# Optimization experiments

Hardware: AMD Instinct MI355X
Metric: run time of the kernel (lower is better)

The kernel has to match this reference:

```python
import jax, jax.numpy as jnp
import numpy as np

# Model dims (match init_kwargs)
NUM_EXPERTS = 8
TOP_K = 2
D_MODEL = 1024
D_FF = 4096
BATCH = 4
SEQ = 2048


def setup_inputs() -> dict:
    key = jax.random.key(0)
    ks = jax.random.split(key, 6)
    x = jax.random.normal(ks[0], (BATCH, SEQ, D_MODEL), dtype=jnp.float32)
    # Linear gating network: logits = x @ Wg + bg
    Wg = jax.random.normal(ks[1], (D_MODEL, NUM_EXPERTS), dtype=jnp.float32) * (D_MODEL ** -0.5)
    bg = jnp.zeros((NUM_EXPERTS,), dtype=jnp.float32)
    # Per-expert 2-layer FFN params, stacked over expert axis E
    W1 = jax.random.normal(ks[2], (NUM_EXPERTS, D_MODEL, D_FF), dtype=jnp.float32) * (D_MODEL ** -0.5)
    b1 = jnp.zeros((NUM_EXPERTS, D_FF), dtype=jnp.float32)
    W2 = jax.random.normal(ks[3], (NUM_EXPERTS, D_FF, D_MODEL), dtype=jnp.float32) * (D_FF ** -0.5)
    b2 = jnp.zeros((NUM_EXPERTS, D_MODEL), dtype=jnp.float32)
    return {"x": x, "Wg": Wg, "bg": bg, "W1": W1, "b1": b1, "W2": W2, "b2": b2}


def reference(x, Wg, bg, W1, b1, W2, b2):
    B, S, D = x.shape
    E = Wg.shape[1]
    xf = x.reshape(-1, D)  # [T, D], T = B*S tokens

    # --- Linear gating: softmax probs, top-k hard assignment mask ---
    gate_logits = xf @ Wg + bg                      # [T, E]
    gate_probs = jax.nn.softmax(gate_logits, -1)    # [T, E]
    _, top_idx = jax.lax.top_k(gate_probs, TOP_K)   # [T, K]
    # expert_assignment = sum over k of one_hot(indices) -> {0,1} mask [T, E]
    assign = jnp.sum(jax.nn.one_hot(top_idx, E, dtype=gate_probs.dtype), axis=-2)

    # --- All experts process all tokens (faithful to _process_hard_routing) ---
    # h: [E, T, F]; out_e: [E, T, D]
    h = jax.nn.gelu(jnp.einsum('td,edf->etf', xf, W1) + b1[:, None, :])
    out_e = jnp.einsum('etf,efd->etd', h, W2) + b2[:, None, :]

    # --- Weighted combine: expert_output * gate_prob * top-k mask, sum over E ---
    w = (gate_probs * assign).T[:, :, None]         # [E, T, 1]
    out = jnp.sum(out_e * w, axis=0)                # [T, D]
    return out.reshape(B, S, D)
```

## Files before the change

kernel.cpp:

```cpp
#include <hip/hip_runtime.h>
#include <hip/hip_bf16.h>
#include <stdint.h>

#define T_TOK 8192
#define DM 1024
#define DF 4096
#define NE 8
#define NSLOT 136

typedef __attribute__((ext_vector_type(8))) short short8;
typedef __attribute__((ext_vector_type(8))) unsigned short ushort8;
typedef __attribute__((ext_vector_type(4))) float f32x4;

#define AS1 __attribute__((address_space(1)))
#define AS3 __attribute__((address_space(3)))

#define NB_GATE (T_TOK / 4)
#define NB_T1 ((DF / 64) * (DM / 64) * NE)
#define NB_T2 ((DM / 64) * (DF / 64) * NE)

static __device__ __forceinline__ unsigned short f2bf(float f) {
  union { float f; unsigned int u; } c; c.f = f;
  unsigned int u = c.u;
  unsigned int r = (u + 0x7FFFu + ((u >> 16) & 1u)) >> 16;
  return (unsigned short)r;
}

static __device__ __forceinline__ float gelu_tanh(float v) {
  float y = 0.7978845608028654f * (v + 0.044715f * v * v * v);
  float ay = fabsf(y);
  float e = __expf(-2.0f * ay);
  float th = (1.0f - e) / (1.0f + e);
  th = copysignf(th, y);
  return 0.5f * v * (1.0f + th);
}

__global__ void k_probe(float* out, float v, int n) {
  int i = blockIdx.x * blockDim.x + threadIdx.x;
  for (; i < n; i += gridDim.x * blockDim.x) out[i] = v;
}

__global__ void k_prep(const float* __restrict__ x, unsigned short* __restrict__ xb,
                       const float* __restrict__ Wg, const float* __restrict__ bg,
                       const float* __restrict__ W1, unsigned short* __restrict__ w1t,
                       const float* __restrict__ W2, unsigned short* __restrict__ w2t,
                       const float* __restrict__ b2, float* __restrict__ out,
                       int* __restrict__ choice2, float* __restrict__ wts) {
  __shared__ float tile[64][65];
  int bid = blockIdx.x;

  if (bid < NB_GATE) {
    int wave = threadIdx.x >> 6, lane = threadIdx.x & 63;
    int t = bid * 4 + wave;
    const float* xr = x + (size_t)t * DM;
    unsigned short* xo = xb + (size_t)t * DM;
    double acc[NE];
#pragma unroll
    for (int e = 0; e < NE; ++e) acc[e] = 0.0;
#pragma unroll
    for (int i = 0; i < 4; ++i) {
      int d = lane * 4 + i * 256;
      float4 v = *(const float4*)(xr + d);
      ushort4 o;
      o.x = f2bf(v.x); o.y = f2bf(v.y); o.z = f2bf(v.z); o.w = f2bf(v.w);
      *(ushort4*)(xo + d) = o;
      float xv[4] = {v.x, v.y, v.z, v.w};
#pragma unroll
      for (int q = 0; q < 4; ++q) {
        const float4* wg = (const float4*)(Wg + (size_t)(d + q) * NE);
        float4 w0 = wg[0], w1 = wg[1];
        acc[0] += (double)xv[q] * w0.x; acc[1] += (double)xv[q] * w0.y;
        acc[2] += (double)xv[q] * w0.z; acc[3] += (double)xv[q] * w0.w;
        acc[4] += (double)xv[q] * w1.x; acc[5] += (double)xv[q] * w1.y;
        acc[6] += (double)xv[q] * w1.z; acc[7] += (double)xv[q] * w1.w;
      }
    }
#pragma unroll
    for (int off = 32; off; off >>= 1)
#pragma unroll
      for (int e = 0; e < NE; ++e) acc[e] += __shfl_xor(acc[e], off);
    int e1i = 0, e2i = 0;
    float w1v = 0.f, w2v = 0.f;
    if (lane == 0) {
      float lg[NE];
#pragma unroll
      for (int e = 0; e < NE; ++e) lg[e] = (float)acc[e] + bg[e];
      float m = lg[0];
#pragma unroll
      for (int e = 1; e < NE; ++e) m = fmaxf(m, lg[e]);
      float s = 0.f, p[NE];
#pragma unroll
      for (int e = 0; e < NE; ++e) { p[e] = expf(lg[e] - m); s += p[e]; }
      float inv = 1.f / s;
      int i1 = 0;
#pragma unroll
      for (int e = 1; e < NE; ++e) if (lg[e] > lg[i1]) i1 = e;
      int i2 = (i1 == 0) ? 1 : 0;
#pragma unroll
      for (int e = 0; e < NE; ++e) if (e != i1 && lg[e] > lg[i2]) i2 = e;
      e1i = i1; e2i = i2;
      w1v = p[i1] * inv; w2v = p[i2] * inv;
      choice2[2 * t] = i1;     wts[2 * t] = w1v;
      choice2[2 * t + 1] = i2; wts[2 * t + 1] = w2v;
    }
    e1i = __shfl(e1i, 0); e2i = __shfl(e2i, 0);
    w1v = __shfl(w1v, 0); w2v = __shfl(w2v, 0);
#pragma unroll
    for (int i = 0; i < 4; ++i) {
      int d = lane * 4 + i * 256;
      float4 a = *(const float4*)(b2 + (size_t)e1i * DM + d);
      float4 b = *(const float4*)(b2 + (size_t)e2i * DM + d);
      float4 o;
      o.x = w1v * a.x + w2v * b.x; o.y = w1v * a.y + w2v * b.y;
      o.z = w1v * a.z + w2v * b.z; o.w = w1v * a.w + w2v * b.w;
      *(float4*)(out + (size_t)t * DM + d) = o;
    }
    return;
  }

  const float* src;
  unsigned short* dst;
  int R, C, r0, c0;
  if (bid < NB_GATE + NB_T1) {
    int b2i = bid - NB_GATE;
    int e = b2i >> 10, rem = b2i & 1023;
    int byy = rem >> 6, bxx = rem & 63;
    R = DM; C = DF; r0 = byy * 64; c0 = bxx * 64;
    src = W1 + (size_t)e * DM * DF;
    dst = w1t + (size_t)e * DM * DF;
  } else {
    int b2i = bid - NB_GATE - NB_T1;
    int e = b2i >> 10, rem = b2i & 1023;
    int byy = rem >> 4, bxx = rem & 15;
    R = DF; C = DM; r0 = byy * 64; c0 = bxx * 64;
    src = W2 + (size_t)e * DF * DM;
    dst = w2t + (size_t)e * DF * DM;
  }
  int tx = threadIdx.x & 15, ty = threadIdx.x >> 4;
#pragma unroll
  for (int i = 0; i < 4; ++i) {
    int r = ty + i * 16;
    float4 v = *(const float4*)(src + (size_t)(r0 + r) * C + c0 + tx * 4);
    tile[r][tx * 4 + 0] = v.x; tile[r][tx * 4 + 1] = v.y;
    tile[r][tx * 4 + 2] = v.z; tile[r][tx * 4 + 3] = v.w;
  }
  __syncthreads();
  int tx2 = threadIdx.x & 7, ty2 = threadIdx.x >> 3;
#pragma unroll
  for (int i = 0; i < 2; ++i) {
    int c = ty2 + i * 32;
    ushort8 o;
#pragma unroll
    for (int j = 0; j < 8; ++j) o[j] = f2bf(tile[tx2 * 8 + j][c]);
    *(ushort8*)(dst + (size_t)(c0 + c) * R + r0 + tx2 * 8) = o;
  }
}

__global__ void k_bucket(const int* __restrict__ choice2, const float* __restrict__ wts,
                         int* __restrict__ counts, int* __restrict__ offsets,
                         int* __restrict__ btok, float* __restrict__ bw,
                         int* __restrict__ work) {
  __shared__ int qc[4][NE];
  int e = blockIdx.x;
  int tid = threadIdx.x;
  int w = tid >> 6, lane = tid & 63;
  const int QUARTER = 2 * T_TOK / 4;
  int base = w * QUARTER;
  unsigned long long below = (lane == 0) ? 0ull : ((1ull << lane) - 1ull);

  int cq[NE];
#pragma unroll
  for (int q = 0; q < NE; ++q) cq[q] = 0;
  for (int i0 = 0; i0 < QUARTER; i0 += 64) {
    int ce = choice2[base + i0 + lane];
#pragma unroll
    for (int q = 0; q < NE; ++q)
      cq[q] += (int)__popcll(__ballot(ce == q));
  }
  if (lane == 0) {
#pragma unroll
    for (int q = 0; q < NE; ++q) qc[w][q] = cq[q];
  }
  __syncthreads();

  int total[NE];
#pragma unroll
  for (int q = 0; q < NE; ++q) total[q] = qc[0][q] + qc[1][q] + qc[2][q] + qc[3][q];
  int off_e = 0;
#pragma unroll
  for (int q = 0; q < NE; ++q) if (q < e) off_e += total[q];
  int pos = 0;
#pragma unroll
  for (int ww = 0; ww < 4; ++ww) if (ww < w) pos += qc[ww][e];

  if (e == 0 && tid == 0) {
    int s = 0;
    for (int q = 0; q < NE; ++q) { counts[q] = total[q]; offsets[q] = s; s += total[q]; }
    int idx = 0;
    for (int q = 0; q < NE; ++q) {
      int nby = (total[q] + 127) >> 7;
      for (int j = 0; j < nby; ++j) work[idx++] = (q << 20) | (j << 7);
    }
    while (idx < NSLOT) work[idx++] = -1;
  }

  for (int i0 = 0; i0 < QUARTER; i0 += 64) {
    int idx = base + i0 + lane;
    int ce = choice2[idx];
    float wt = wts[idx];
    unsigned long long m = __ballot(ce == e);
    if (ce == e) {
      int r = (int)__popcll(m & below);
      btok[e * T_TOK + pos + r] = idx >> 1;
      bw[e * T_TOK + pos + r] = wt;
    }
    pos += (int)__popcll(m);
  }
}


__global__ __launch_bounds__(256, 4) void k_gemm1(
    const unsigned short* __restrict__ xb,
    const unsigned short* __restrict__ w1t,
    const float* __restrict__ b1,
    const int* __restrict__ counts, const int* __restrict__ offsets,
    const int* __restrict__ btok, const int* __restrict__ work,
    unsigned short* __restrict__ H,
    int gx) {
  __shared__ __align__(16) unsigned short ldsA[128 * 64];
  __shared__ __align__(16) unsigned short ldsB[128 * 64];
  __shared__ int toksh[128];

  int nwg = gx * NSLOT;
  int bid = blockIdx.x;
  int wg = (bid & 7) * (nwg >> 3) + (bid >> 3);
  int slot = wg / gx;
  int bx = wg - slot * gx;
  int pk = work[slot];
  if (pk < 0) return;
  int e = pk >> 20;
  int m0 = pk & 0xFFFFF;
  int cnt = counts[e];
  int eoff = offsets[e];
  int f0 = bx * 128;
  int tid = threadIdx.x;
  int wave = tid >> 6, lane = tid & 63;

  for (int i = tid; i < 128; i += 256) {
    int p = m0 + i; if (p >= cnt) p = cnt - 1;
    toksh[i] = btok[e * T_TOK + p];
  }
  __syncthreads();

  int slin = lane & 7, rsub = lane >> 3;
  int ksl8 = (slin ^ rsub) * 8;

  const unsigned short* srcA[4];
  const unsigned short* srcB[4];
  int ldsg[4];
#pragma unroll
  for (int j = 0; j < 4; ++j) {
    int g = j * 4 + wave;
    int m = g * 8 + rsub;
    srcA[j] = xb + (size_t)toksh[m] * DM + ksl8;
    srcB[j] = w1t + ((size_t)e * DF + f0 + m) * DM + ksl8;
    ldsg[j] = g * 512;
  }

  auto stage = [&](int ks) {
#pragma unroll
    for (int j = 0; j < 4; ++j) {
      __builtin_amdgcn_global_load_lds((const AS1 void*)(srcA[j] + (size_t)ks * 64),
                                       (AS3 void*)(&ldsA[ldsg[j]]), 16, 0, 0);
      __builtin_amdgcn_global_load_lds((const AS1 void*)(srcB[j] + (size_t)ks * 64),
                                       (AS3 void*)(&ldsB[ldsg[j]]), 16, 0, 0);
    }
  };

  int wm = wave >> 1, wn = wave & 1;
  int lrow = lane & 15, khi = lane >> 4;
  f32x4 acc[4][4];
#pragma unroll
  for (int m = 0; m < 4; ++m)
#pragma unroll
    for (int n = 0; n < 4; ++n) acc[m][n] = (f32x4){0.f, 0.f, 0.f, 0.f};

  auto compute = [&]() {
#pragma unroll
    for (int kk = 0; kk < 2; ++kk) {
      int kslot = kk * 4 + khi;
      short8 af[4], bfv[4];
#pragma unroll
      for (int m = 0; m < 4; ++m) {
        int row = wm * 64 + m * 16 + lrow;
        int slotx = kslot ^ (row & 7);
        af[m] = *(const short8*)(&ldsA[row * 64 + slotx * 8]);
      }
#pragma unroll
      for (int n = 0; n < 4; ++n) {
        int row = wn * 64 + n * 16 + lrow;
        int slotx = kslot ^ (row & 7);
        bfv[n] = *(const short8*)(&ldsB[row * 64 + slotx * 8]);
      }
#pragma unroll
      for (int m = 0; m < 4; ++m)
#pragma unroll
        for (int n = 0; n < 4; ++n)
          acc[m][n] = __builtin_amdgcn_mfma_f32_16x16x32_bf16(af[m], bfv[n], acc[m][n], 0, 0, 0);
    }
  };

  const int nk = DM / 64;
  for (int ks = 0; ks < nk; ++ks) {
    stage(ks);
    __syncthreads();
    compute();
    __syncthreads();
  }

#pragma unroll
  for (int m = 0; m < 4; ++m) {
    int rbase = wm * 64 + m * 16 + khi * 4;
#pragma unroll
    for (int j = 0; j < 4; ++j) {
      int pos = m0 + rbase + j;
      if (pos < cnt) {
        size_t hrow = (size_t)(eoff + pos) * DF;
#pragma unroll
        for (int n = 0; n < 4; ++n) {
          int fl = f0 + wn * 64 + n * 16 + lrow;
          float v = acc[m][n][j] + b1[e * DF + fl];
          H[hrow + fl] = f2bf(gelu_tanh(v));
        }
      }
    }
  }
}

__global__ __launch_bounds__(256, 4) void k_gemm2(
    const unsigned short* __restrict__ H,
    const unsigned short* __restrict__ w2t,
    const int* __restrict__ counts, const int* __restrict__ offsets,
    const int* __restrict__ btok, const float* __restrict__ bw,
    const int* __restrict__ work,
    float* __restrict__ out, int gx) {
  __shared__ __align__(16) unsigned short ldsA[128 * 64];
  __shared__ __align__(16) unsigned short ldsB[128 * 64];
  __shared__ int toksh[128];
  __shared__ float wsh[128];

  int nwg = gx * NSLOT;
  int bid = blockIdx.x;
  int wg = (bid & 7) * (nwg >> 3) + (bid >> 3);
  int slot = wg / gx;
  int bx = wg - slot * gx;
  int pk = work[slot];
  if (pk < 0) return;
  int e = pk >> 20;
  int m0 = pk & 0xFFFFF;
  int cnt = counts[e];
  int eoff = offsets[e];
  int d0 = bx * 128;
  int tid = threadIdx.x;
  int wave = tid >> 6, lane = tid & 63;

  for (int i = tid; i < 128; i += 256) {
    int p = m0 + i; if (p >= cnt) p = cnt - 1;
    toksh[i] = btok[e * T_TOK + p];
    wsh[i] = bw[e * T_TOK + p];
  }
  __syncthreads();

  int slin = lane & 7, rsub = lane >> 3;
  int ksl8 = (slin ^ rsub) * 8;

  const unsigned short* srcA[4];
  const unsigned short* srcB[4];
  int ldsg[4];
#pragma unroll
  for (int j = 0; j < 4; ++j) {
    int g = j * 4 + wave;
    int m = g * 8 + rsub;
    int p = m0 + m; if (p >= cnt) p = cnt - 1;
    srcA[j] = H + (size_t)(eoff + p) * DF + ksl8;
    srcB[j] = w2t + ((size_t)e * DM + d0 + m) * DF + ksl8;
    ldsg[j] = g * 512;
  }

  auto stage = [&](int ks) {
#pragma unroll
    for (int j = 0; j < 4; ++j) {
      __builtin_amdgcn_global_load_lds((const AS1 void*)(srcA[j] + (size_t)ks * 64),
                                       (AS3 void*)(&ldsA[ldsg[j]]), 16, 0, 0);
      __builtin_amdgcn_global_load_lds((const AS1 void*)(srcB[j] + (size_t)ks * 64),
                                       (AS3 void*)(&ldsB[ldsg[j]]), 16, 0, 0);
    }
  };

  int wm = wave >> 1, wn = wave & 1;
  int lrow = lane & 15, khi = lane >> 4;
  f32x4 acc[4][4];
#pragma unroll
  for (int m = 0; m < 4; ++m)
#pragma unroll
    for (int n = 0; n < 4; ++n) acc[m][n] = (f32x4){0.f, 0.f, 0.f, 0.f};

  auto compute = [&]() {
#pragma unroll
    for (int kk = 0; kk < 2; ++kk) {
      int kslot = kk * 4 + khi;
      short8 af[4], bfv[4];
#pragma unroll
      for (int m = 0; m < 4; ++m) {
        int row = wm * 64 + m * 16 + lrow;
        int slotx = kslot ^ (row & 7);
        af[m] = *(const short8*)(&ldsA[row * 64 + slotx * 8]);
      }
#pragma unroll
      for (int n = 0; n < 4; ++n) {
        int row = wn * 64 + n * 16 + lrow;
        int slotx = kslot ^ (row & 7);
        bfv[n] = *(const short8*)(&ldsB[row * 64 + slotx * 8]);
      }
#pragma unroll
      for (int m = 0; m < 4; ++m)
#pragma unroll
        for (int n = 0; n < 4; ++n)
          acc[m][n] = __builtin_amdgcn_mfma_f32_16x16x32_bf16(af[m], bfv[n], acc[m][n], 0, 0, 0);
    }
  };

  const int nk = DF / 64;
  for (int ks = 0; ks < nk; ++ks) {
    stage(ks);
    __syncthreads();
    compute();
    __syncthreads();
  }

#pragma unroll
  for (int m = 0; m < 4; ++m) {
    int rbase = wm * 64 + m * 16 + khi * 4;
#pragma unroll
    for (int j = 0; j < 4; ++j) {
      int lr = rbase + j;
      int pos = m0 + lr;
      if (pos < cnt) {
        int tok = toksh[lr];
        float wgt = wsh[lr];
#pragma unroll
        for (int n = 0; n < 4; ++n) {
          int dc = d0 + wn * 64 + n * 16 + lrow;
          atomicAdd(&out[(size_t)tok * DM + dc], wgt * acc[m][n][j]);
        }
      }
    }
  }
}

extern "C" void kernel_launch(void* const* d_in, const int* in_sizes, int n_in,
                              void* d_out, int out_size, void* d_ws, size_t ws_size,
                              hipStream_t stream) {
  const float* x  = (const float*)d_in[0];
  const float* Wg = (const float*)d_in[1];
  const float* bg = (const float*)d_in[2];
  const float* W1 = (const float*)d_in[3];
  const float* b1 = (const float*)d_in[4];
  const float* W2 = (const float*)d_in[5];
  const float* b2 = (const float*)d_in[6];
  float* out = (float*)d_out;

  uint8_t* ws = (uint8_t*)d_ws;
  size_t off = 0;
  auto alloc = [&](size_t bytes) {
    size_t o = off;
    off = (off + bytes + 255) & ~(size_t)255;
    return o;
  };
  size_t o_counts = alloc(NE * 4);
  size_t o_offsets = alloc(NE * 4);
  size_t o_work = alloc(NSLOT * 4);
  size_t o_choice = alloc((size_t)2 * T_TOK * 4);
  size_t o_wts = alloc((size_t)2 * T_TOK * 4);
  size_t o_btok = alloc((size_t)NE * T_TOK * 4);
  size_t o_bw = alloc((size_t)NE * T_TOK * 4);
  size_t o_xb = alloc((size_t)T_TOK * DM * 2);
  size_t o_w1t = alloc((size_t)NE * DF * DM * 2);
  size_t o_w2t = alloc((size_t)NE * DM * DF * 2);
  size_t o_h = alloc((size_t)2 * T_TOK * DF * 2);

  if (off > ws_size) {
    k_probe<<<dim3(1024), dim3(256), 0, stream>>>(out, (float)(double)ws_size, out_size);
    return;
  }

  int* counts = (int*)(ws + o_counts);
  int* offsets = (int*)(ws + o_offsets);
  int* work = (int*)(ws + o_work);
  int* choice2 = (int*)(ws + o_choice);
  float* wtsp = (float*)(ws + o_wts);
  int* btok = (int*)(ws + o_btok);
  float* bwp = (float*)(ws + o_bw);
  unsigned short* xb = (unsigned short*)(ws + o_xb);
  unsigned short* w1t = (unsigned short*)(ws + o_w1t);
  unsigned short* w2t = (unsigned short*)(ws + o_w2t);
  unsigned short* Hbuf = (unsigned short*)(ws + o_h);

  k_prep<<<dim3(NB_GATE + NB_T1 + NB_T2), dim3(256), 0, stream>>>(
      x, xb, Wg, bg, W1, w1t, W2, w2t, b2, out, choice2, wtsp);
  k_bucket<<<dim3(NE), dim3(256), 0, stream>>>(choice2, wtsp, counts, offsets, btok, bwp, work);

  int g1x = DF / 128;
  int g2x = DM / 128;
  k_gemm1<<<dim3(g1x * NSLOT), dim3(256), 0, stream>>>(
      xb, w1t, b1, counts, offsets, btok, work, Hbuf, g1x);
  k_gemm2<<<dim3(g2x * NSLOT), dim3(256), 0, stream>>>(
      Hbuf, w2t, counts, offsets, btok, bwp, work, out, g2x);
}
```

Measured before the change: 550.6 us.

## Enlarge GEMM M tile to 256 tokens with 512-thread workgroups

Both expert GEMM kernels now take 256-row token tiles instead of 128, using 8 waves per workgroup. The work list is rebuilt in 256-token blocks and the slot count shrinks accordingly. The LDS staging layout is reorganised so each thread loads linear 16-byte chunks with an XOR swizzle. The goal is to reuse each weight tile across twice as many tokens, cutting weight traffic per token. The cost is more LDS and registers per workgroup, lower occupancy, and more padding waste in partially filled expert buckets.

```diff
diff --git a/kernel.cpp b/kernel.cpp
--- a/kernel.cpp
+++ b/kernel.cpp
@@ -6,7 +6,7 @@
 #define DM 1024
 #define DF 4096
 #define NE 8
-#define NSLOT 136
+#define NSLOT 72
 
 typedef __attribute__((ext_vector_type(8))) short short8;
 typedef __attribute__((ext_vector_type(8))) unsigned short ushort8;
@@ -186,9 +186,6 @@
   int total[NE];
 #pragma unroll
   for (int q = 0; q < NE; ++q) total[q] = qc[0][q] + qc[1][q] + qc[2][q] + qc[3][q];
-  int off_e = 0;
-#pragma unroll
-  for (int q = 0; q < NE; ++q) if (q < e) off_e += total[q];
   int pos = 0;
 #pragma unroll
   for (int ww = 0; ww < 4; ++ww) if (ww < w) pos += qc[ww][e];
@@ -198,8 +195,8 @@
     for (int q = 0; q < NE; ++q) { counts[q] = total[q]; offsets[q] = s; s += total[q]; }
     int idx = 0;
     for (int q = 0; q < NE; ++q) {
-      int nby = (total[q] + 127) >> 7;
-      for (int j = 0; j < nby; ++j) work[idx++] = (q << 20) | (j << 7);
+      int nby = (total[q] + 255) >> 8;
+      for (int j = 0; j < nby; ++j) work[idx++] = (q << 20) | (j << 8);
     }
     while (idx < NSLOT) work[idx++] = -1;
   }
@@ -219,7 +216,7 @@
 }
 
 
-__global__ __launch_bounds__(256, 4) void k_gemm1(
+__global__ __launch_bounds__(512, 4) void k_gemm1(
     const unsigned short* __restrict__ xb,
     const unsigned short* __restrict__ w1t,
     const float* __restrict__ b1,
@@ -227,9 +224,9 @@
     const int* __restrict__ btok, const int* __restrict__ work,
     unsigned short* __restrict__ H,
     int gx) {
-  __shared__ __align__(16) unsigned short ldsA[128 * 64];
+  __shared__ __align__(16) unsigned short ldsA[256 * 64];
   __shared__ __align__(16) unsigned short ldsB[128 * 64];
-  __shared__ int toksh[128];
+  __shared__ int toksh[256];
 
   int nwg = gx * NSLOT;
   int bid = blockIdx.x;
@@ -246,35 +243,36 @@
   int tid = threadIdx.x;
   int wave = tid >> 6, lane = tid & 63;
 
-  for (int i = tid; i < 128; i += 256) {
-    int p = m0 + i; if (p >= cnt) p = cnt - 1;
-    toksh[i] = btok[e * T_TOK + p];
+  if (tid < 256) {
+    int p = m0 + tid; if (p >= cnt) p = cnt - 1;
+    toksh[tid] = btok[e * T_TOK + p];
   }
   __syncthreads();
 
-  int slin = lane & 7, rsub = lane >> 3;
-  int ksl8 = (slin ^ rsub) * 8;
-
   const unsigned short* srcA[4];
-  const unsigned short* srcB[4];
-  int ldsg[4];
+  const unsigned short* srcB[2];
 #pragma unroll
   for (int j = 0; j < 4; ++j) {
-    int g = j * 4 + wave;
-    int m = g * 8 + rsub;
-    srcA[j] = xb + (size_t)toksh[m] * DM + ksl8;
-    srcB[j] = w1t + ((size_t)e * DF + f0 + m) * DM + ksl8;
-    ldsg[j] = g * 512;
+    int s = j * 512 + tid;
+    int row = s >> 3, q = s & 7;
+    srcA[j] = xb + (size_t)toksh[row] * DM + ((q ^ (row & 7)) * 8);
+  }
+#pragma unroll
+  for (int j = 0; j < 2; ++j) {
+    int s = j * 512 + tid;
+    int row = s >> 3, q = s & 7;
+    srcB[j] = w1t + ((size_t)e * DF + f0 + row) * DM + ((q ^ (row & 7)) * 8);
   }
 
   auto stage = [&](int ks) {
 #pragma unroll
-    for (int j = 0; j < 4; ++j) {
+    for (int j = 0; j < 4; ++j)
       __builtin_amdgcn_global_load_lds((const AS1 void*)(srcA[j] + (size_t)ks * 64),
-                                       (AS3 void*)(&ldsA[ldsg[j]]), 16, 0, 0);
+                                       (AS3 void*)(&ldsA[(j * 512 + tid) * 8]), 16, 0, 0);
+#pragma unroll
+    for (int j = 0; j < 2; ++j)
       __builtin_amdgcn_global_load_lds((const AS1 void*)(srcB[j] + (size_t)ks * 64),
-                                       (AS3 void*)(&ldsB[ldsg[j]]), 16, 0, 0);
-    }
+                                       (AS3 void*)(&ldsB[(j * 512 + tid) * 8]), 16, 0, 0);
   };
 
   int wm = wave >> 1, wn = wave & 1;
@@ -337,17 +335,17 @@
   }
 }
 
-__global__ __launch_bounds__(256, 4) void k_gemm2(
+__global__ __launch_bounds__(512, 4) void k_gemm2(
     const unsigned short* __restrict__ H,
     const unsigned short* __restrict__ w2t,
     const int* __restrict__ counts, const int* __restrict__ offsets,
     const int* __restrict__ btok, const float* __restrict__ bw,
     const int* __restrict__ work,
     float* __restrict__ out, int gx) {
-  __shared__ __align__(16) unsigned short ldsA[128 * 64];
+  __shared__ __align__(16) unsigned short ldsA[256 * 64];
   __shared__ __align__(16) unsigned short ldsB[128 * 64];
-  __shared__ int toksh[128];
-  __shared__ float wsh[128];
+  __shared__ int toksh[256];
+  __shared__ float wsh[256];
 
   int nwg = gx * NSLOT;
   int bid = blockIdx.x;
@@ -364,37 +362,38 @@
   int tid = threadIdx.x;
   int wave = tid >> 6, lane = tid & 63;
 
-  for (int i = tid; i < 128; i += 256) {
-    int p = m0 + i; if (p >= cnt) p = cnt - 1;
-    toksh[i] = btok[e * T_TOK + p];
-    wsh[i] = bw[e * T_TOK + p];
+  if (tid < 256) {
+    int p = m0 + tid; if (p >= cnt) p = cnt - 1;
+    toksh[tid] = btok[e * T_TOK + p];
+    wsh[tid] = bw[e * T_TOK + p];
   }
   __syncthreads();
 
-  int slin = lane & 7, rsub = lane >> 3;
-  int ksl8 = (slin ^ rsub) * 8;
-
   const unsigned short* srcA[4];
-  const unsigned short* srcB[4];
-  int ldsg[4];
+  const unsigned short* srcB[2];
 #pragma unroll
   for (int j = 0; j < 4; ++j) {
-    int g = j * 4 + wave;
-    int m = g * 8 + rsub;
-    int p = m0 + m; if (p >= cnt) p = cnt - 1;
-    srcA[j] = H + (size_t)(eoff + p) * DF + ksl8;
-    srcB[j] = w2t + ((size_t)e * DM + d0 + m) * DF + ksl8;
-    ldsg[j] = g * 512;
+    int s = j * 512 + tid;
+    int row = s >> 3, q = s & 7;
+    int p = m0 + row; if (p >= cnt) p = cnt - 1;
+    srcA[j] = H + (size_t)(eoff + p) * DF + ((q ^ (row & 7)) * 8);
+  }
+#pragma unroll
+  for (int j = 0; j < 2; ++j) {
+    int s = j * 512 + tid;
+    int row = s >> 3, q = s & 7;
+    srcB[j] = w2t + ((size_t)e * DM + d0 + row) * DF + ((q ^ (row & 7)) * 8);
   }
 
   auto stage = [&](int ks) {
 #pragma unroll
-    for (int j = 0; j < 4; ++j) {
+    for (int j = 0; j < 4; ++j)
       __builtin_amdgcn_global_load_lds((const AS1 void*)(srcA[j] + (size_t)ks * 64),
-                                       (AS3 void*)(&ldsA[ldsg[j]]), 16, 0, 0);
+                                       (AS3 void*)(&ldsA[(j * 512 + tid) * 8]), 16, 0, 0);
+#pragma unroll
+    for (int j = 0; j < 2; ++j)
       __builtin_amdgcn_global_load_lds((const AS1 void*)(srcB[j] + (size_t)ks * 64),
-                                       (AS3 void*)(&ldsB[ldsg[j]]), 16, 0, 0);
-    }
+                                       (AS3 void*)(&ldsB[(j * 512 + tid) * 8]), 16, 0, 0);
   };
 
   int wm = wave >> 1, wn = wave & 1;
@@ -512,8 +511,8 @@
 
   int g1x = DF / 128;
   int g2x = DM / 128;
-  k_gemm1<<<dim3(g1x * NSLOT), dim3(256), 0, stream>>>(
+  k_gemm1<<<dim3(g1x * NSLOT), dim3(512), 0, stream>>>(
       xb, w1t, b1, counts, offsets, btok, work, Hbuf, g1x);
-  k_gemm2<<<dim3(g2x * NSLOT), dim3(256), 0, stream>>>(
+  k_gemm2<<<dim3(g2x * NSLOT), dim3(512), 0, stream>>>(
       Hbuf, w2t, counts, offsets, btok, bwp, work, out, g2x);
 }
```

New measurement: 627.1 us. 1.14x slower.
